# Performance work log

Measured on AMD Instinct MI355X. Metric: run time of the kernel, lower is better.

## Reference

```python
import jax, jax.numpy as jnp
import numpy as np

B, N, D, R = 2, 256, 128, 32

def _sh_l1(r):
    # e3nn-style component-normalized l=1 spherical harmonics of unit vectors
    return jnp.sqrt(3.0) * r

def _sh_l2(r):
    x, y, z = r[..., 0], r[..., 1], r[..., 2]
    c = jnp.sqrt(15.0)
    return jnp.stack([
        c * x * y,
        c * y * z,
        0.5 * jnp.sqrt(5.0) * (3.0 * z * z - 1.0),  # x^2+y^2+z^2 = 1
        c * x * z,
        0.5 * c * (x * x - y * y),
    ], axis=-1)

def _radial(rbf, w1, b1, w2, b2):
    h = rbf @ w1 + b1
    return (h * jax.nn.sigmoid(h)) @ w2 + b2  # Linear -> SiLU -> Linear

def _layernorm(x, g, b, eps=1e-5):
    m = jnp.mean(x, axis=-1, keepdims=True)
    v = jnp.var(x, axis=-1, keepdims=True)
    return (x - m) * jax.lax.rsqrt(v + eps) * g + b

def setup_inputs() -> dict:
    key = jax.random.key(0)
    ks = iter(jax.random.split(key, 40))
    def nrm(shape, s=1.0):
        return jax.random.normal(next(ks), shape, dtype=jnp.float32) * s
    r_hat = nrm((B, N, N, 3))
    r_hat = r_hat / (jnp.linalg.norm(r_hat, axis=-1, keepdims=True) + 1e-9)
    inp = {
        'node_s': nrm((B, N, D)),
        'node_v': nrm((B, N, 3, D)),
        'node_t': nrm((B, N, 5, D)),
        'rbf': jax.random.uniform(next(ks), (B, N, N, R), dtype=jnp.float32),
        'r_hat': r_hat,
        'mask': jnp.ones((B, N, N), dtype=jnp.float32),
    }
    s1, s2 = 1.0 / np.sqrt(R), 1.0 / np.sqrt(D)
    for p in ('r0', 'r1', 'r2', 'r110'):
        inp[p + '_w1'] = nrm((R, D), s1)
        inp[p + '_b1'] = jnp.zeros((D,), jnp.float32)
        inp[p + '_w2'] = nrm((D, D), s2)
        inp[p + '_b2'] = jnp.zeros((D,), jnp.float32)
    inp['src_w'] = nrm((D, D), s2)
    inp['ln_g'] = jnp.ones((D,), jnp.float32)
    inp['ln_b'] = jnp.zeros((D,), jnp.float32)
    inp['out_w'] = nrm((D, D), s2)
    inp['out_b'] = jnp.zeros((D,), jnp.float32)
    inp['v_scale'] = jnp.ones((D,), jnp.float32)
    inp['t_scale'] = jnp.ones((D,), jnp.float32)
    return inp

def reference(node_s, node_v, node_t, rbf, r_hat, mask,
              r0_w1, r0_b1, r0_w2, r0_b2,
              r1_w1, r1_b1, r1_w2, r1_b2,
              r2_w1, r2_b1, r2_w2, r2_b2,
              r110_w1, r110_b1, r110_w2, r110_b2,
              src_w, ln_g, ln_b, out_w, out_b, v_scale, t_scale):
    h = node_s @ src_w                               # (B,N,D)
    h_j = h[:, None, :, :] * mask[..., None]         # (B,N,N,D): h_j[b,i,j]=h[b,j]*mask[b,i,j]
    Y1 = _sh_l1(r_hat)                               # (B,N,N,3)
    Y2 = _sh_l2(r_hat)                               # (B,N,N,5)

    msg_s = jnp.sum(h_j * _radial(rbf, r0_w1, r0_b1, r0_w2, r0_b2), axis=2)  # (B,N,D)
    delta_v = jnp.einsum('bijd,bijc->bicd',
                         h_j * _radial(rbf, r1_w1, r1_b1, r1_w2, r1_b2), Y1) * v_scale
    delta_t = jnp.einsum('bijd,bijc->bicd',
                         h_j * _radial(rbf, r2_w1, r2_b1, r2_w2, r2_b2), Y2) * t_scale

    # v_j[b,i,j] = node_v[b,i] (per the torch unsqueeze(2).expand)
    dot_vY1 = jnp.einsum('bicd,bijc->bijd', node_v, Y1)                      # (B,N,N,D)
    msg_s_from_v = jnp.sum(dot_vY1 * _radial(rbf, r110_w1, r110_b1, r110_w2, r110_b2)
                           * mask[..., None], axis=2)                        # (B,N,D)

    delta_s = _layernorm(msg_s + msg_s_from_v, ln_g, ln_b) @ out_w + out_b
    return (delta_s, delta_v, delta_t)
```

## Files before the change

kernel.cpp:

```cpp
#include <hip/hip_runtime.h>

#define Bb 2
#define Nn 256
#define Dd 128
#define Rr 32

typedef unsigned short u16;
typedef unsigned int   u32;
typedef __attribute__((ext_vector_type(8))) short bf16x8;
typedef __attribute__((ext_vector_type(4))) float f32x4;
typedef __attribute__((ext_vector_type(2))) u32   u32x2;
typedef __attribute__((ext_vector_type(4))) u32   u32x4;

__device__ u16 g_w1t[4*Dd*Rr];
__device__ u16 g_w2t[4*Dd*Dd];

__device__ __forceinline__ short f2bfs(float f){
  u32 u = __float_as_uint(f);
  u += 0x7FFFu + ((u >> 16) & 1u);
  return (short)(u >> 16);
}
__device__ __forceinline__ u16 f2bf(float f){
  u32 u = __float_as_uint(f);
  u += 0x7FFFu + ((u >> 16) & 1u);
  return (u16)(u >> 16);
}
__device__ __forceinline__ u32 cvtpk(float a, float b){
  u32 r;
  asm("v_cvt_pk_bf16_f32 %0, %1, %2" : "=v"(r) : "v"(a), "v"(b));
  return r;
}

__global__ __launch_bounds__(128) void prep_kernel(
    const float* __restrict__ node_s, const float* __restrict__ src_w,
    const float* __restrict__ r0w1, const float* __restrict__ r1w1,
    const float* __restrict__ r2w1, const float* __restrict__ r3w1,
    const float* __restrict__ r0w2, const float* __restrict__ r1w2,
    const float* __restrict__ r2w2, const float* __restrict__ r3w2,
    float* __restrict__ h_out)
{
  const int bx = blockIdx.x;
  const int t  = threadIdx.x;
  if (bx < Bb*Nn){
    __shared__ float s_row[Dd];
    s_row[t] = node_s[(size_t)bx*Dd + t];
    __syncthreads();
    float acc = 0.f;
    #pragma unroll 8
    for (int k=0;k<Dd;k++) acc += s_row[k]*src_w[k*Dd + t];
    const int b = bx >> 8, i = bx & 255;
    h_out[(size_t)(b*Dd + t)*Nn + i] = acc;
  } else {
    const int kb = bx - Bb*Nn;
    const int p  = kb >> 3, sl = kb & 7;
    const float* W1 = (p==0)?r0w1:(p==1)?r1w1:(p==2)?r2w1:r3w1;
    const float* W2 = (p==0)?r0w2:(p==1)?r1w2:(p==2)?r2w2:r3w2;
    u16* W1T = g_w1t + p*Dd*Rr;
    u16* W2T = g_w2t + p*Dd*Dd;
    #pragma unroll
    for (int it=0; it<4; it++){
      int in = sl*512 + it*128 + t;
      W1T[(in & 127)*Rr + (in >> 7)] = f2bf(W1[in]);
    }
    #pragma unroll
    for (int it=0; it<16; it++){
      int in = sl*2048 + it*128 + t;
      W2T[(in & 127)*Dd + (in >> 7)] = f2bf(W2[in]);
    }
  }
}

__global__ __launch_bounds__(512,4) void se3_mfma17(
    const float* __restrict__ node_v,
    const float* __restrict__ rbf,
    const float* __restrict__ r_hat,
    const float* __restrict__ maskp,
    const float* __restrict__ r0b1, const float* __restrict__ r0b2,
    const float* __restrict__ r1b1, const float* __restrict__ r1b2,
    const float* __restrict__ r2b1, const float* __restrict__ r2b2,
    const float* __restrict__ r3b1, const float* __restrict__ r3b2,
    const float* __restrict__ ln_g, const float* __restrict__ ln_b,
    const float* __restrict__ out_w, const float* __restrict__ out_b,
    const float* __restrict__ v_scale, const float* __restrict__ t_scale,
    const float* __restrict__ h_ws,
    float* __restrict__ out_s, float* __restrict__ out_v, float* __restrict__ out_t)
{
  __shared__ u16   s_rbf[Nn*40];
  __shared__ u16   s_hid[2*64*130];
  __shared__ u16   s_YT[11*264];
  __shared__ u16   s_Y1r[3*264];
  __shared__ float s_msg[Dd];
  __shared__ float s_xn[Dd];
  __shared__ float s_part[4*Dd];
  __shared__ float s_mv[2];

  const int tid  = threadIdx.x;
  const int bi   = blockIdx.x;
  const int b    = bi >> 8;
  const int lane = tid & 63;
  const int w    = tid >> 6;
  const int q    = lane >> 4;
  const int cc   = lane & 15;
  const int hi5  = cc >> 2, lo2 = cc & 3;
  const int dwb  = w*16;

  if (tid < Nn){
    int j = tid;
    size_t pidx = (size_t)bi*Nn + j;
    float mk = maskp[pidx];
    float x = r_hat[pidx*3+0];
    float y = r_hat[pidx*3+1];
    float z = r_hat[pidx*3+2];
    const float SQ3=1.7320508075688772f;
    const float C15=3.8729833462074170f;
    const float C5H=1.1180339887498949f;
    float y1a=SQ3*x, y1b=SQ3*y, y1c=SQ3*z;
    s_YT[0*264+j]=f2bf(mk);
    s_YT[1*264+j]=f2bf(y1a*mk);
    s_YT[2*264+j]=f2bf(y1b*mk);
    s_YT[3*264+j]=f2bf(y1c*mk);
    s_YT[4*264+j]=f2bf(C15*x*y*mk);
    s_YT[5*264+j]=f2bf(C15*y*z*mk);
    s_YT[6*264+j]=f2bf(C5H*(3.f*z*z-1.f)*mk);
    s_YT[7*264+j]=f2bf(C15*x*z*mk);
    s_YT[8*264+j]=f2bf(0.5f*C15*(x*x-y*y)*mk);
    s_YT[9*264+j]=f2bf(mk);
    s_YT[10*264+j]=0;
    s_Y1r[0*264+j]=f2bf(y1a);
    s_Y1r[1*264+j]=f2bf(y1b);
    s_Y1r[2*264+j]=f2bf(y1c);
  }

  const float* rbf_blk = rbf + (size_t)bi*Nn*Rr;
  const float* htb     = h_ws + (size_t)b*Dd*Nn;

  for (int idx=tid; idx<Nn*Rr/2; idx+=512){
    int j = idx >> 4, r2 = (idx & 15)*2;
    const float* src = &rbf_blk[j*Rr + r2];
    float v0 = src[0], v1 = src[1];
    *(u32*)&s_rbf[j*40 + r2] = cvtpk(v0, v1);
  }

  bf16x8 vBf;
  {
    const float* nv = node_v + (size_t)bi*3*Dd;
    int dd = dwb+cc;
    bf16x8 t = {0,0,0,0,0,0,0,0};
    if (q==0){
      t[0]=f2bfs(nv[0*Dd+dd]);
      t[1]=f2bfs(nv[1*Dd+dd]);
      t[2]=f2bfs(nv[2*Dd+dd]);
    }
    vBf=t;
  }

  const int rbf_base = cc*40 + q*8;
  const int hw_base  = cc*130 + w*16 + q*4;
  const int af_base  = (hi5*8+lo2)*130 + q*8;

  __syncthreads();

  const f32x4 zf = {0.f,0.f,0.f,0.f};
  f32x4 accred = zf;

  bf16x8 w1f;  f32x4 b1v4;
  bf16x8 w2f[4]; float b2v;
  const u16* ytq;

  auto do_gemm1 = [&](int rb, int bufn){
    #pragma unroll
    for (int jt=0;jt<4;jt++){
      bf16x8 rbff = *(const bf16x8*)&s_rbf[rbf_base + rb + jt*640];
      f32x4 hc = __builtin_amdgcn_mfma_f32_16x16x32_bf16(w1f, rbff, zf, 0,0,0);
      float s0,s1,s2,s3;
      {
        float x0=hc[0]+b1v4[0], x1=hc[1]+b1v4[1], x2=hc[2]+b1v4[2], x3=hc[3]+b1v4[3];
        s0 = x0*__builtin_amdgcn_rcpf(1.f+__expf(-x0));
        s1 = x1*__builtin_amdgcn_rcpf(1.f+__expf(-x1));
        s2 = x2*__builtin_amdgcn_rcpf(1.f+__expf(-x2));
        s3 = x3*__builtin_amdgcn_rcpf(1.f+__expf(-x3));
      }
      u32x2 pk = { cvtpk(s0, s1), cvtpk(s2, s3) };
      *(u32x2*)&s_hid[bufn*8320 + hw_base + jt*2080] = pk;
    }
  };

  auto do_gemm2 = [&](int choff, int bufx, int p){
    f32x4 hql[2][2];
    if (p<3){
      #pragma unroll
      for (int g=0;g<2;g++)
        #pragma unroll
        for (int mm=0;mm<2;mm++)
          hql[g][mm] = *(const f32x4*)&htb[(size_t)(dwb+cc)*Nn + choff + g*32 + q*8 + mm*4];
    }
    #pragma unroll
    for (int g=0; g<2; g++){
      u32 bB[4];
      #pragma unroll
      for (int mm=0;mm<2;mm++){
        bf16x8 af[4];
        #pragma unroll
        for (int ks=0;ks<4;ks++)
          af[ks] = *(const bf16x8*)&s_hid[bufx*8320 + af_base + g*4160 + mm*520 + ks*32];

        f32x4 dotC;
        if (p==3){
          bf16x8 aY = {0,0,0,0,0,0,0,0};
          if (q==0){
            int jg = choff + g*32 + hi5*8 + mm*4 + lo2;
            aY[0]=(short)s_Y1r[0*264+jg];
            aY[1]=(short)s_Y1r[1*264+jg];
            aY[2]=(short)s_Y1r[2*264+jg];
          }
          dotC = __builtin_amdgcn_mfma_f32_16x16x32_bf16(aY, vBf, zf, 0,0,0);
        }

        f32x4 c2 = zf;
        #pragma unroll
        for (int ks=0;ks<4;ks++)
          c2 = __builtin_amdgcn_mfma_f32_16x16x32_bf16(af[ks], w2f[ks], c2, 0,0,0);
        float g0,g1,g2,g3;
        if (p<3){
          g0=(c2[0]+b2v)*hql[0][0][0], g1=(c2[1]+b2v)*hql[0][0][1];
          g0=(c2[0]+b2v)*hql[g][mm][0]; g1=(c2[1]+b2v)*hql[g][mm][1];
          g2=(c2[2]+b2v)*hql[g][mm][2]; g3=(c2[3]+b2v)*hql[g][mm][3];
        } else {
          g0=(c2[0]+b2v)*dotC[0]; g1=(c2[1]+b2v)*dotC[1];
          g2=(c2[2]+b2v)*dotC[2]; g3=(c2[3]+b2v)*dotC[3];
        }
        bB[mm*2+0] = cvtpk(g0, g1);
        bB[mm*2+1] = cvtpk(g2, g3);
      }
      bf16x8 aR = *(const bf16x8*)(ytq + choff + g*32);
      u32x4 bw = { bB[0], bB[1], bB[2], bB[3] };
      bf16x8 bG = __builtin_bit_cast(bf16x8, bw);
      accred = __builtin_amdgcn_mfma_f32_16x16x32_bf16(aR, bG, accred, 0,0,0);
    }
  };

  w1f  = *(const bf16x8*)&g_w1t[(dwb+cc)*Rr + q*8];
  b1v4 = *(const f32x4*)&r0b1[dwb + q*4];
  do_gemm1(0, 0);

  #pragma unroll 1
  for (int p=0;p<4;p++){
    {
      const u16* W2T = g_w2t + p*Dd*Dd;
      #pragma unroll
      for (int ks=0;ks<4;ks++)
        w2f[ks] = *(const bf16x8*)&W2T[(dwb+cc)*Dd + ks*32 + q*8];
      const float* B2p = (p==0)?r0b2:(p==1)?r1b2:(p==2)?r2b2:r3b2;
      b2v = B2p[dwb + cc];
      const int lo = (p==0)?0:(p==1)?1:(p==2)?4:9;
      const int hi = (p==0)?0:(p==1)?3:(p==2)?8:9;
      ytq = &s_YT[((cc>=lo && cc<=hi)?cc:10)*264] + q*8;
    }
    #pragma unroll 1
    for (int u=0; u<2; u++){
      const int rb0   = u*5120;
      const int choff = u*128;
      __syncthreads();
      do_gemm1(rb0 + 2560, 1);
      do_gemm2(choff, 0, p);
      __syncthreads();
      if (u==0){
        do_gemm1(rb0 + 5120, 0);
      } else if (p<3){
        w1f  = *(const bf16x8*)&g_w1t[(p+1)*Dd*Rr + (dwb+cc)*Rr + q*8];
        const float* B1n = (p==0)?r1b1:(p==1)?r2b1:r3b1;
        b1v4 = *(const f32x4*)&B1n[dwb + q*4];
        do_gemm1(0, 0);
      }
      do_gemm2(choff + 64, 1, p);
    }
  }

  {
    const int d = dwb + cc;
    #pragma unroll
    for (int r=0;r<4;r++){
      const int rw = q*4 + r;
      float val = accred[r];
      if (rw==0)      s_msg[d] = val;
      else if (rw<=3) out_v[(size_t)bi*3*Dd + (size_t)(rw-1)*Dd + d] = val*v_scale[d];
      else if (rw<=8) out_t[(size_t)bi*5*Dd + (size_t)(rw-4)*Dd + d] = val*t_scale[d];
      else if (rw==9) s_xn[d] = val;
    }
  }
  __syncthreads();

  if (tid < 64){
    float a0=s_msg[tid]+s_xn[tid], a1=s_msg[tid+64]+s_xn[tid+64];
    float s1=a0+a1, s2=a0*a0+a1*a1;
    #pragma unroll
    for (int off=1;off<64;off<<=1){
      s1 += __shfl_xor(s1,off);
      s2 += __shfl_xor(s2,off);
    }
    if (tid==0){
      float m   = s1*(1.f/Dd);
      float var = fmaxf(s2*(1.f/Dd) - m*m, 0.f);
      s_mv[0]=m;
      s_mv[1]=rsqrtf(var+1e-5f);
    }
  }
  __syncthreads();
  if (tid < Dd){
    float msg = s_msg[tid]+s_xn[tid];
    s_xn[tid] = (msg - s_mv[0])*s_mv[1]*ln_g[tid] + ln_b[tid];
  }
  __syncthreads();

  {
    int dp = tid & 127, seg = tid >> 7;
    float pa = 0.f;
    #pragma unroll 8
    for (int k=seg*32;k<seg*32+32;k++)
      pa += s_xn[k]*out_w[k*Dd+dp];
    s_part[seg*Dd+dp]=pa;
  }
  __syncthreads();
  if (tid < Dd)
    out_s[(size_t)bi*Dd+tid] = s_part[tid]+s_part[Dd+tid]+s_part[2*Dd+tid]+s_part[3*Dd+tid]+out_b[tid];
}

extern "C" void kernel_launch(void* const* d_in, const int* in_sizes, int n_in,
                              void* d_out, int out_size, void* d_ws, size_t ws_size,
                              hipStream_t stream) {
  const float* node_s = (const float*)d_in[0];
  const float* node_v = (const float*)d_in[1];
  const float* rbf    = (const float*)d_in[3];
  const float* r_hat  = (const float*)d_in[4];
  const float* maskp  = (const float*)d_in[5];
  const float* r0w1=(const float*)d_in[6],  *r0b1=(const float*)d_in[7];
  const float* r0w2=(const float*)d_in[8],  *r0b2=(const float*)d_in[9];
  const float* r1w1=(const float*)d_in[10], *r1b1=(const float*)d_in[11];
  const float* r1w2=(const float*)d_in[12], *r1b2=(const float*)d_in[13];
  const float* r2w1=(const float*)d_in[14], *r2b1=(const float*)d_in[15];
  const float* r2w2=(const float*)d_in[16], *r2b2=(const float*)d_in[17];
  const float* r3w1=(const float*)d_in[18], *r3b1=(const float*)d_in[19];
  const float* r3w2=(const float*)d_in[20], *r3b2=(const float*)d_in[21];
  const float* src_w  =(const float*)d_in[22];
  const float* ln_g   =(const float*)d_in[23];
  const float* ln_b   =(const float*)d_in[24];
  const float* out_w  =(const float*)d_in[25];
  const float* out_b  =(const float*)d_in[26];
  const float* v_scale=(const float*)d_in[27];
  const float* t_scale=(const float*)d_in[28];

  float* h_ws = (float*)d_ws;
  float* out_s = (float*)d_out;
  float* out_v = out_s + (size_t)Bb*Nn*Dd;
  float* out_t = out_v + (size_t)Bb*Nn*3*Dd;

  prep_kernel<<<dim3(Bb*Nn + 32), dim3(128), 0, stream>>>(
      node_s, src_w,
      r0w1, r1w1, r2w1, r3w1, r0w2, r1w2, r2w2, r3w2,
      h_ws);
  se3_mfma17<<<dim3(Bb*Nn), dim3(512), 0, stream>>>(
      node_v, rbf, r_hat, maskp,
      r0b1,r0b2, r1b1,r1b2, r2b1,r2b2, r3b1,r3b2,
      ln_g, ln_b, out_w, out_b, v_scale, t_scale,
      h_ws, out_s, out_v, out_t);
}
```

Baseline: 178.7 us.

## Split GEMM2 work across wave pairs by j-half with 32-wide d tiles

Each wave pair now covers 32 output channels, and each wave handles one half of the 64 j-rows per chunk instead of all j-rows for 16 channels. Every A-fragment loaded from shared memory now feeds two N-tiles, which halves the s_hid reads per MFMA. The partial reductions from the two halves are combined through a new shared buffer plus an extra barrier. The cost is more registers (two sets of W2 fragments and two accumulators) under launch_bounds(512,4), and some added LDS use.

```diff
diff --git a/kernel.cpp b/kernel.cpp
--- a/kernel.cpp
+++ b/kernel.cpp
@@ -70,7 +70,7 @@
   }
 }
 
-__global__ __launch_bounds__(512,4) void se3_mfma17(
+__global__ __launch_bounds__(512,4) void se3_mfma18(
     const float* __restrict__ node_v,
     const float* __restrict__ rbf,
     const float* __restrict__ r_hat,
@@ -89,6 +89,7 @@
   __shared__ u16   s_hid[2*64*130];
   __shared__ u16   s_YT[11*264];
   __shared__ u16   s_Y1r[3*264];
+  __shared__ float s_red[16*130];
   __shared__ float s_msg[Dd];
   __shared__ float s_xn[Dd];
   __shared__ float s_part[4*Dd];
@@ -103,6 +104,8 @@
   const int cc   = lane & 15;
   const int hi5  = cc >> 2, lo2 = cc & 3;
   const int dwb  = w*16;
+  const int pwb  = (w>>1)*32;
+  const int half = w & 1;
 
   if (tid < Nn){
     int j = tid;
@@ -141,30 +144,33 @@
     *(u32*)&s_rbf[j*40 + r2] = cvtpk(v0, v1);
   }
 
-  bf16x8 vBf;
+  bf16x8 vBf[2];
   {
     const float* nv = node_v + (size_t)bi*3*Dd;
-    int dd = dwb+cc;
-    bf16x8 t = {0,0,0,0,0,0,0,0};
-    if (q==0){
-      t[0]=f2bfs(nv[0*Dd+dd]);
-      t[1]=f2bfs(nv[1*Dd+dd]);
-      t[2]=f2bfs(nv[2*Dd+dd]);
-    }
-    vBf=t;
+    #pragma unroll
+    for (int nt=0;nt<2;nt++){
+      int dd = pwb + nt*16 + cc;
+      bf16x8 t = {0,0,0,0,0,0,0,0};
+      if (q==0){
+        t[0]=f2bfs(nv[0*Dd+dd]);
+        t[1]=f2bfs(nv[1*Dd+dd]);
+        t[2]=f2bfs(nv[2*Dd+dd]);
+      }
+      vBf[nt]=t;
+    }
   }
 
   const int rbf_base = cc*40 + q*8;
   const int hw_base  = cc*130 + w*16 + q*4;
-  const int af_base  = (hi5*8+lo2)*130 + q*8;
+  const int af_base  = (half*32 + hi5*8 + lo2)*130 + q*8;
 
   __syncthreads();
 
   const f32x4 zf = {0.f,0.f,0.f,0.f};
-  f32x4 accred = zf;
+  f32x4 accred[2] = {zf, zf};
 
   bf16x8 w1f;  f32x4 b1v4;
-  bf16x8 w2f[4]; float b2v;
+  bf16x8 w2f[2][4]; float b2v[2];
   const u16* ytq;
 
   auto do_gemm1 = [&](int rb, int bufn){
@@ -186,56 +192,59 @@
   };
 
   auto do_gemm2 = [&](int choff, int bufx, int p){
-    f32x4 hql[2][2];
-    if (p<3){
-      #pragma unroll
-      for (int g=0;g<2;g++)
+    u32 bB[2][4];
+    #pragma unroll
+    for (int mm=0;mm<2;mm++){
+      bf16x8 af[4];
+      #pragma unroll
+      for (int ks=0;ks<4;ks++)
+        af[ks] = *(const bf16x8*)&s_hid[bufx*8320 + af_base + mm*520 + ks*32];
+
+      f32x4 hq[2];
+      if (p<3){
         #pragma unroll
-        for (int mm=0;mm<2;mm++)
-          hql[g][mm] = *(const f32x4*)&htb[(size_t)(dwb+cc)*Nn + choff + g*32 + q*8 + mm*4];
-    }
-    #pragma unroll
-    for (int g=0; g<2; g++){
-      u32 bB[4];
-      #pragma unroll
-      for (int mm=0;mm<2;mm++){
-        bf16x8 af[4];
+        for (int nt=0;nt<2;nt++)
+          hq[nt] = *(const f32x4*)&htb[(size_t)(pwb+nt*16+cc)*Nn + choff + half*32 + q*8 + mm*4];
+      }
+
+      f32x4 dotC[2];
+      if (p==3){
+        bf16x8 aY = {0,0,0,0,0,0,0,0};
+        if (q==0){
+          int jg = choff + half*32 + hi5*8 + mm*4 + lo2;
+          aY[0]=(short)s_Y1r[0*264+jg];
+          aY[1]=(short)s_Y1r[1*264+jg];
+          aY[2]=(short)s_Y1r[2*264+jg];
+        }
         #pragma unroll
-        for (int ks=0;ks<4;ks++)
-          af[ks] = *(const bf16x8*)&s_hid[bufx*8320 + af_base + g*4160 + mm*520 + ks*32];
-
-        f32x4 dotC;
-        if (p==3){
-          bf16x8 aY = {0,0,0,0,0,0,0,0};
-          if (q==0){
-            int jg = choff + g*32 + hi5*8 + mm*4 + lo2;
-            aY[0]=(short)s_Y1r[0*264+jg];
-            aY[1]=(short)s_Y1r[1*264+jg];
-            aY[2]=(short)s_Y1r[2*264+jg];
-          }
-          dotC = __builtin_amdgcn_mfma_f32_16x16x32_bf16(aY, vBf, zf, 0,0,0);
-        }
-
+        for (int nt=0;nt<2;nt++)
+          dotC[nt] = __builtin_amdgcn_mfma_f32_16x16x32_bf16(aY, vBf[nt], zf, 0,0,0);
+      }
+
+      #pragma unroll
+      for (int nt=0;nt<2;nt++){
         f32x4 c2 = zf;
         #pragma unroll
         for (int ks=0;ks<4;ks++)
-          c2 = __builtin_amdgcn_mfma_f32_16x16x32_bf16(af[ks], w2f[ks], c2, 0,0,0);
+          c2 = __builtin_amdgcn_mfma_f32_16x16x32_bf16(af[ks], w2f[nt][ks], c2, 0,0,0);
         float g0,g1,g2,g3;
         if (p<3){
-          g0=(c2[0]+b2v)*hql[0][0][0], g1=(c2[1]+b2v)*hql[0][0][1];
-          g0=(c2[0]+b2v)*hql[g][mm][0]; g1=(c2[1]+b2v)*hql[g][mm][1];
-          g2=(c2[2]+b2v)*hql[g][mm][2]; g3=(c2[3]+b2v)*hql[g][mm][3];
+          g0=(c2[0]+b2v[nt])*hq[nt][0]; g1=(c2[1]+b2v[nt])*hq[nt][1];
+          g2=(c2[2]+b2v[nt])*hq[nt][2]; g3=(c2[3]+b2v[nt])*hq[nt][3];
         } else {
-          g0=(c2[0]+b2v)*dotC[0]; g1=(c2[1]+b2v)*dotC[1];
-          g2=(c2[2]+b2v)*dotC[2]; g3=(c2[3]+b2v)*dotC[3];
+          g0=(c2[0]+b2v[nt])*dotC[nt][0]; g1=(c2[1]+b2v[nt])*dotC[nt][1];
+          g2=(c2[2]+b2v[nt])*dotC[nt][2]; g3=(c2[3]+b2v[nt])*dotC[nt][3];
         }
-        bB[mm*2+0] = cvtpk(g0, g1);
-        bB[mm*2+1] = cvtpk(g2, g3);
-      }
-      bf16x8 aR = *(const bf16x8*)(ytq + choff + g*32);
-      u32x4 bw = { bB[0], bB[1], bB[2], bB[3] };
+        bB[nt][mm*2+0] = cvtpk(g0, g1);
+        bB[nt][mm*2+1] = cvtpk(g2, g3);
+      }
+    }
+    bf16x8 aR = *(const bf16x8*)(ytq + choff + half*32);
+    #pragma unroll
+    for (int nt=0;nt<2;nt++){
+      u32x4 bw = { bB[nt][0], bB[nt][1], bB[nt][2], bB[nt][3] };
       bf16x8 bG = __builtin_bit_cast(bf16x8, bw);
-      accred = __builtin_amdgcn_mfma_f32_16x16x32_bf16(aR, bG, accred, 0,0,0);
+      accred[nt] = __builtin_amdgcn_mfma_f32_16x16x32_bf16(aR, bG, accred[nt], 0,0,0);
     }
   };
 
@@ -247,11 +256,15 @@
   for (int p=0;p<4;p++){
     {
       const u16* W2T = g_w2t + p*Dd*Dd;
-      #pragma unroll
-      for (int ks=0;ks<4;ks++)
-        w2f[ks] = *(const bf16x8*)&W2T[(dwb+cc)*Dd + ks*32 + q*8];
       const float* B2p = (p==0)?r0b2:(p==1)?r1b2:(p==2)?r2b2:r3b2;
-      b2v = B2p[dwb + cc];
+      #pragma unroll
+      for (int nt=0;nt<2;nt++){
+        int dd = pwb + nt*16 + cc;
+        #pragma unroll
+        for (int ks=0;ks<4;ks++)
+          w2f[nt][ks] = *(const bf16x8*)&W2T[dd*Dd + ks*32 + q*8];
+        b2v[nt] = B2p[dd];
+      }
       const int lo = (p==0)?0:(p==1)?1:(p==2)?4:9;
       const int hi = (p==0)?0:(p==1)?3:(p==2)?8:9;
       ytq = &s_YT[((cc>=lo && cc<=hi)?cc:10)*264] + q*8;
@@ -276,16 +289,29 @@
     }
   }
 
-  {
-    const int d = dwb + cc;
-    #pragma unroll
-    for (int r=0;r<4;r++){
-      const int rw = q*4 + r;
-      float val = accred[r];
-      if (rw==0)      s_msg[d] = val;
-      else if (rw<=3) out_v[(size_t)bi*3*Dd + (size_t)(rw-1)*Dd + d] = val*v_scale[d];
-      else if (rw<=8) out_t[(size_t)bi*5*Dd + (size_t)(rw-4)*Dd + d] = val*t_scale[d];
-      else if (rw==9) s_xn[d] = val;
+  if (half){
+    #pragma unroll
+    for (int nt=0;nt<2;nt++){
+      const int d = pwb + nt*16 + cc;
+      #pragma unroll
+      for (int r=0;r<4;r++)
+        s_red[(q*4+r)*130 + d] = accred[nt][r];
+    }
+  }
+  __syncthreads();
+  if (!half){
+    #pragma unroll
+    for (int nt=0;nt<2;nt++){
+      const int d = pwb + nt*16 + cc;
+      #pragma unroll
+      for (int r=0;r<4;r++){
+        const int rw = q*4 + r;
+        float val = accred[nt][r] + s_red[rw*130 + d];
+        if (rw==0)      s_msg[d] = val;
+        else if (rw<=3) out_v[(size_t)bi*3*Dd + (size_t)(rw-1)*Dd + d] = val*v_scale[d];
+        else if (rw<=8) out_t[(size_t)bi*5*Dd + (size_t)(rw-4)*Dd + d] = val*t_scale[d];
+        else if (rw==9) s_xn[d] = val;
+      }
     }
   }
   __syncthreads();
@@ -358,7 +384,7 @@
       node_s, src_w,
       r0w1, r1w1, r2w1, r3w1, r0w2, r1w2, r2w2, r3w2,
       h_ws);
-  se3_mfma17<<<dim3(Bb*Nn), dim3(512), 0, stream>>>(
+  se3_mfma18<<<dim3(Bb*Nn), dim3(512), 0, stream>>>(
       node_v, rbf, r_hat, maskp,
       r0b1,r0b2, r1b1,r1b2, r2b1,r2b2, r3b1,r3b2,
       ln_g, ln_b, out_w, out_b, v_scale, t_scale,
```

Result: slower. 186.0 us (+4.1%).
